# Kernel optimization log

Hardware: AMD Instinct MI355X
Metric: run time of the kernel (lower is better)

The kernel has to match this reference:

```python
import jax, jax.numpy as jnp
import numpy as np

N = 8192
D_IN = 512
D_OUT = 512


def setup_inputs() -> dict:
    key = jax.random.key(0)
    k1, k2, k3, k4 = jax.random.split(key, 4)
    x = jax.random.normal(k1, (N, D_IN), dtype=jnp.float32)
    adj = jax.random.uniform(k2, (N, N), dtype=jnp.float32)
    # nn.Linear params: weight (out, in), bias (out,)
    bound = 1.0 / np.sqrt(D_IN)
    W = jax.random.uniform(k3, (D_OUT, D_IN), minval=-bound, maxval=bound, dtype=jnp.float32)
    b = jax.random.uniform(k4, (D_OUT,), minval=-bound, maxval=bound, dtype=jnp.float32)
    return {"x": x, "adj": adj, "W": W, "b": b}


def reference(x, adj, W, b):
    # Symmetric normalization: D^-1/2 (A + I) D^-1/2.
    # Original uses diag-matmuls; broadcast scaling is the identical math
    # without the O(n^3) diagonal GEMMs.
    a = adj + jnp.eye(adj.shape[0], dtype=adj.dtype)
    d = jnp.sum(a, axis=1) ** -0.5  # (N,)
    a_norm = d[:, None] * a * d[None, :]
    support = a_norm @ x                      # (N, D_IN)
    out = support @ W.T + b                   # (N, D_OUT)
    out = jax.nn.relu(out)
    # dropout: identity in eval/reference mode
    return out
```

## Files before the change

### kernel.cpp

```cpp
#include <hip/hip_runtime.h>
#include <stdint.h>

typedef __bf16 bf16_t;
typedef __bf16 bf16x8 __attribute__((ext_vector_type(8)));
typedef __bf16 bf16x4v __attribute__((ext_vector_type(4)));
typedef float f32x16 __attribute__((ext_vector_type(16)));

#define AS_GLOBAL __attribute__((address_space(1)))
#define AS_LDS    __attribute__((address_space(3)))

static constexpr int NN   = 8192;
static constexpr int DIN  = 512;
static constexpr int DOUT = 512;
static constexpr int SPLITK = 2;

__device__ __forceinline__ void async_cp16(const bf16_t* g, bf16_t* l) {
  __builtin_amdgcn_global_load_lds((AS_GLOBAL unsigned int*)g,
                                   (AS_LDS unsigned int*)l, 16, 0, 0);
}

__global__ __launch_bounds__(256) void k_rowsum_convert(
    const float* __restrict__ adj, bf16_t* __restrict__ adjb,
    float* __restrict__ d) {
  const int row = blockIdx.x;
  const int t = threadIdx.x;
  const float4* rf4 = (const float4*)(adj + (size_t)row * NN);
  bf16_t* outp = adjb + (size_t)row * NN;
  float sum = 0.f;
#pragma unroll
  for (int c = 0; c < 8; ++c) {
    int f4i = c * 256 + t;
    float4 a = rf4[f4i];
    sum += a.x + a.y + a.z + a.w;
    bf16x4v o;
    o[0] = (bf16_t)a.x; o[1] = (bf16_t)a.y; o[2] = (bf16_t)a.z; o[3] = (bf16_t)a.w;
    *(bf16x4v*)(outp + f4i * 4) = o;
  }
#pragma unroll
  for (int off = 32; off > 0; off >>= 1) sum += __shfl_down(sum, off);
  __shared__ float red[4];
  if ((t & 63) == 0) red[t >> 6] = sum;
  __syncthreads();
  if (t == 0) {
    float s = red[0] + red[1] + red[2] + red[3] + 1.0f;
    d[row] = rsqrtf(s);
  }
}

__global__ __launch_bounds__(256) void k_make_xsT(
    const float* __restrict__ x, const float* __restrict__ d,
    bf16_t* __restrict__ xsT) {
  __shared__ bf16_t T[64][72];
  const int t = threadIdx.x;
  const int k0 = blockIdx.x * 64, j0 = blockIdx.y * 64;
#pragma unroll
  for (int it = 0; it < 4; ++it) {
    int idx = it * 256 + t;
    int r = idx >> 4, c = idx & 15;
    float4 v = *(const float4*)(x + (size_t)(k0 + r) * DIN + j0 + c * 4);
    float s = d[k0 + r];
    T[r][c * 4 + 0] = (bf16_t)(v.x * s);
    T[r][c * 4 + 1] = (bf16_t)(v.y * s);
    T[r][c * 4 + 2] = (bf16_t)(v.z * s);
    T[r][c * 4 + 3] = (bf16_t)(v.w * s);
  }
  __syncthreads();
#pragma unroll
  for (int it = 0; it < 2; ++it) {
    int idx = it * 256 + t;
    int j = idx >> 3, kb = idx & 7;
    bf16x8 o;
#pragma unroll
    for (int e = 0; e < 8; ++e) o[e] = T[kb * 8 + e][j];
    *(bf16x8*)(xsT + (size_t)(j0 + j) * NN + k0 + kb * 8) = o;
  }
}

__global__ __launch_bounds__(256) void k_convert_w(
    const float* __restrict__ W, bf16_t* __restrict__ Wb) {
  int idx = blockIdx.x * 256 + threadIdx.x;
  float4 v = *(const float4*)(W + (size_t)idx * 4);
  bf16x4v o;
  o[0] = (bf16_t)v.x; o[1] = (bf16_t)v.y; o[2] = (bf16_t)v.z; o[3] = (bf16_t)v.w;
  *(bf16x4v*)(Wb + (size_t)idx * 4) = o;
}

__device__ __forceinline__ void gemm_tile_128x128(
    const bf16_t* __restrict__ A, const bf16_t* __restrict__ B,
    int lda, int ldb, int m0, int n0, int kStart, int kEnd,
    bf16_t* As, bf16_t* Bs, f32x16 acc[2][2]) {
  const int t = threadIdx.x;
  const int lane = t & 63;
  const int wid = t >> 6;
  const int wm = wid >> 1, wn = wid & 1;
  const int l32 = lane & 31, half = lane >> 5;

  const int swz = (t & 7) ^ ((t >> 3) & 7);
  const bf16_t* gA = A + (size_t)(m0 + (t >> 3)) * lda + swz * 8 + kStart;
  const bf16_t* gB = B + (size_t)(n0 + (t >> 3)) * ldb + swz * 8 + kStart;
  bf16_t* lA = As + t * 8;
  bf16_t* lB = Bs + t * 8;

  const int xorc = lane & 7;

  for (int k0 = kStart; k0 < kEnd; k0 += 64) {
#pragma unroll
    for (int i = 0; i < 4; ++i) {
      async_cp16(gA + (size_t)(i * 32) * lda, lA + i * 2048);
      async_cp16(gB + (size_t)(i * 32) * ldb, lB + i * 2048);
    }
    gA += 64; gB += 64;
    __syncthreads();
#pragma unroll
    for (int ks = 0; ks < 4; ++ks) {
      const int pchunk = ((ks * 2 + half) ^ xorc) * 8;
      bf16x8 av[2], bv[2];
#pragma unroll
      for (int f = 0; f < 2; ++f) {
        av[f] = *(const bf16x8*)(As + (wm * 64 + f * 32 + l32) * 64 + pchunk);
        bv[f] = *(const bf16x8*)(Bs + (wn * 64 + f * 32 + l32) * 64 + pchunk);
      }
#pragma unroll
      for (int fm = 0; fm < 2; ++fm)
#pragma unroll
        for (int fn = 0; fn < 2; ++fn)
          acc[fm][fn] = __builtin_amdgcn_mfma_f32_32x32x16_bf16(
              av[fm], bv[fn], acc[fm][fn], 0, 0, 0);
    }
    __syncthreads();
  }
}

__global__ __launch_bounds__(256) void k_gemm1(
    const bf16_t* __restrict__ adjb, const bf16_t* __restrict__ xsT,
    float* __restrict__ part) {
  __shared__ bf16_t As[128 * 64];
  __shared__ bf16_t Bs[128 * 64];
  f32x16 acc[2][2];
#pragma unroll
  for (int a = 0; a < 2; ++a)
#pragma unroll
    for (int b = 0; b < 2; ++b)
#pragma unroll
      for (int r = 0; r < 16; ++r) acc[a][b][r] = 0.f;

  const int m0 = blockIdx.x * 128, n0 = blockIdx.y * 128;
  const int kc = blockIdx.z;
  const int kChunk = NN / SPLITK;
  gemm_tile_128x128(adjb, xsT, NN, NN, m0, n0, kc * kChunk, (kc + 1) * kChunk,
                    As, Bs, acc);

  const int t = threadIdx.x;
  const int lane = t & 63, wid = t >> 6;
  const int wm = wid >> 1, wn = wid & 1;
  const int l32 = lane & 31, half = lane >> 5;
  float* outp = part + (size_t)kc * NN * DIN;
#pragma unroll
  for (int fm = 0; fm < 2; ++fm)
#pragma unroll
    for (int fn = 0; fn < 2; ++fn) {
      int gc = n0 + wn * 64 + fn * 32 + l32;
#pragma unroll
      for (int reg = 0; reg < 16; ++reg) {
        int gr = m0 + wm * 64 + fm * 32 + (reg & 3) + 8 * (reg >> 2) + 4 * half;
        outp[(size_t)gr * DIN + gc] = acc[fm][fn][reg];
      }
    }
}

__global__ __launch_bounds__(256) void k_combine(
    const float* __restrict__ part, const float* __restrict__ d,
    const float* __restrict__ x, bf16_t* __restrict__ supB) {
  int idx = blockIdx.x * 256 + threadIdx.x;
  int i = idx >> 7;
  float4 p = *(const float4*)(part + (size_t)idx * 4);
#pragma unroll
  for (int kc = 1; kc < SPLITK; ++kc) {
    float4 q = *(const float4*)(part + (size_t)kc * NN * DIN + (size_t)idx * 4);
    p.x += q.x; p.y += q.y; p.z += q.z; p.w += q.w;
  }
  float4 xv = *(const float4*)(x + (size_t)idx * 4);
  float di = d[i];
  float dii = di * di;
  bf16x4v o;
  o[0] = (bf16_t)(di * p.x + dii * xv.x);
  o[1] = (bf16_t)(di * p.y + dii * xv.y);
  o[2] = (bf16_t)(di * p.z + dii * xv.z);
  o[3] = (bf16_t)(di * p.w + dii * xv.w);
  *(bf16x4v*)(supB + (size_t)idx * 4) = o;
}

__global__ __launch_bounds__(256) void k_gemm2(
    const bf16_t* __restrict__ supB, const bf16_t* __restrict__ Wb,
    const float* __restrict__ bias, float* __restrict__ outp) {
  __shared__ bf16_t As[128 * 64];
  __shared__ bf16_t Bs[128 * 64];
  f32x16 acc[2][2];
#pragma unroll
  for (int a = 0; a < 2; ++a)
#pragma unroll
    for (int b = 0; b < 2; ++b)
#pragma unroll
      for (int r = 0; r < 16; ++r) acc[a][b][r] = 0.f;

  const int m0 = blockIdx.x * 128, n0 = blockIdx.y * 128;
  gemm_tile_128x128(supB, Wb, DIN, DIN, m0, n0, 0, DIN, As, Bs, acc);

  const int t = threadIdx.x;
  const int lane = t & 63, wid = t >> 6;
  const int wm = wid >> 1, wn = wid & 1;
  const int l32 = lane & 31, half = lane >> 5;
#pragma unroll
  for (int fn = 0; fn < 2; ++fn) {
    int gc = n0 + wn * 64 + fn * 32 + l32;
    float bb = bias[gc];
#pragma unroll
    for (int fm = 0; fm < 2; ++fm)
#pragma unroll
      for (int reg = 0; reg < 16; ++reg) {
        int gr = m0 + wm * 64 + fm * 32 + (reg & 3) + 8 * (reg >> 2) + 4 * half;
        float v = acc[fm][fn][reg] + bb;
        outp[(size_t)gr * DOUT + gc] = v > 0.f ? v : 0.f;
      }
  }
}

extern "C" void kernel_launch(void* const* d_in, const int* in_sizes, int n_in,
                              void* d_out, int out_size, void* d_ws, size_t ws_size,
                              hipStream_t stream) {
  const float* x   = (const float*)d_in[0];
  const float* adj = (const float*)d_in[1];
  const float* W   = (const float*)d_in[2];
  const float* b   = (const float*)d_in[3];
  float* out = (float*)d_out;

  char* ws = (char*)d_ws;
  bf16_t* adjb = (bf16_t*)(ws);
  float*  part = (float*)(ws + 134217728);
  size_t  off  = 134217728 + (size_t)SPLITK * NN * DIN * 4;
  bf16_t* xsT  = (bf16_t*)(ws + off);
  bf16_t* supB = (bf16_t*)(ws + off + 8388608);
  bf16_t* Wb   = (bf16_t*)(ws + off + 16777216);
  float*  dvec = (float*)(ws + off + 17301504);

  k_rowsum_convert<<<NN, 256, 0, stream>>>(adj, adjb, dvec);
  k_make_xsT<<<dim3(NN / 64, DIN / 64), 256, 0, stream>>>(x, dvec, xsT);
  k_convert_w<<<(DOUT * DIN) / 1024, 256, 0, stream>>>(W, Wb);
  k_gemm1<<<dim3(NN / 128, DIN / 128, SPLITK), 256, 0, stream>>>(adjb, xsT, part);
  k_combine<<<(NN * DIN) / 1024, 256, 0, stream>>>(part, dvec, x, supB);
  k_gemm2<<<dim3(NN / 128, DOUT / 128), 256, 0, stream>>>(supB, Wb, b, out);
}
```

Baseline: 519.7 us.

## Reassociate GCN as A·(D·X·Wᵀ), fold identity into adj, double-buffer GEMM

Reorders the computation so X·Wᵀ, scaled by the degree vector, is computed first as a small GEMM. The result is written transposed and fed to the big adjacency GEMM. The identity diagonal is folded into the bf16 adjacency during conversion, and bias plus ReLU move into the split-K reduction kernel. This removes the separate x transpose kernel and the second N×512×512 GEMM over the support matrix. It also adds LDS double-buffering with explicit vmcnt waits to both GEMMs. The trade-off is that rounding now happens at different points and LDS use per block doubles.

```diff
diff --git a/kernel.cpp b/kernel.cpp
--- a/kernel.cpp
+++ b/kernel.cpp
@@ -26,6 +26,7 @@
   const int t = threadIdx.x;
   const float4* rf4 = (const float4*)(adj + (size_t)row * NN);
   bf16_t* outp = adjb + (size_t)row * NN;
+  const int diagF4 = row >> 2;
   float sum = 0.f;
 #pragma unroll
   for (int c = 0; c < 8; ++c) {
@@ -34,6 +35,11 @@
     sum += a.x + a.y + a.z + a.w;
     bf16x4v o;
     o[0] = (bf16_t)a.x; o[1] = (bf16_t)a.y; o[2] = (bf16_t)a.z; o[3] = (bf16_t)a.w;
+    if (f4i == diagF4) {
+      int s = row & 3;
+      float vv = s == 0 ? a.x : s == 1 ? a.y : s == 2 ? a.z : a.w;
+      o[s] = (bf16_t)(vv + 1.0f);
+    }
     *(bf16x4v*)(outp + f4i * 4) = o;
   }
 #pragma unroll
@@ -47,33 +53,17 @@
   }
 }
 
-__global__ __launch_bounds__(256) void k_make_xsT(
+__global__ __launch_bounds__(256) void k_dx(
     const float* __restrict__ x, const float* __restrict__ d,
-    bf16_t* __restrict__ xsT) {
-  __shared__ bf16_t T[64][72];
-  const int t = threadIdx.x;
-  const int k0 = blockIdx.x * 64, j0 = blockIdx.y * 64;
-#pragma unroll
-  for (int it = 0; it < 4; ++it) {
-    int idx = it * 256 + t;
-    int r = idx >> 4, c = idx & 15;
-    float4 v = *(const float4*)(x + (size_t)(k0 + r) * DIN + j0 + c * 4);
-    float s = d[k0 + r];
-    T[r][c * 4 + 0] = (bf16_t)(v.x * s);
-    T[r][c * 4 + 1] = (bf16_t)(v.y * s);
-    T[r][c * 4 + 2] = (bf16_t)(v.z * s);
-    T[r][c * 4 + 3] = (bf16_t)(v.w * s);
-  }
-  __syncthreads();
-#pragma unroll
-  for (int it = 0; it < 2; ++it) {
-    int idx = it * 256 + t;
-    int j = idx >> 3, kb = idx & 7;
-    bf16x8 o;
-#pragma unroll
-    for (int e = 0; e < 8; ++e) o[e] = T[kb * 8 + e][j];
-    *(bf16x8*)(xsT + (size_t)(j0 + j) * NN + k0 + kb * 8) = o;
-  }
+    bf16_t* __restrict__ dxb) {
+  int idx = blockIdx.x * 256 + threadIdx.x;
+  int i = idx >> 7;
+  float4 v = *(const float4*)(x + (size_t)idx * 4);
+  float s = d[i];
+  bf16x4v o;
+  o[0] = (bf16_t)(v.x * s); o[1] = (bf16_t)(v.y * s);
+  o[2] = (bf16_t)(v.z * s); o[3] = (bf16_t)(v.w * s);
+  *(bf16x4v*)(dxb + (size_t)idx * 4) = o;
 }
 
 __global__ __launch_bounds__(256) void k_convert_w(
@@ -85,7 +75,7 @@
   *(bf16x4v*)(Wb + (size_t)idx * 4) = o;
 }
 
-__device__ __forceinline__ void gemm_tile_128x128(
+__device__ __forceinline__ void gemm_tile_128x128_db(
     const bf16_t* __restrict__ A, const bf16_t* __restrict__ B,
     int lda, int ldb, int m0, int n0, int kStart, int kEnd,
     bf16_t* As, bf16_t* Bs, f32x16 acc[2][2]) {
@@ -98,27 +88,42 @@
   const int swz = (t & 7) ^ ((t >> 3) & 7);
   const bf16_t* gA = A + (size_t)(m0 + (t >> 3)) * lda + swz * 8 + kStart;
   const bf16_t* gB = B + (size_t)(n0 + (t >> 3)) * ldb + swz * 8 + kStart;
-  bf16_t* lA = As + t * 8;
-  bf16_t* lB = Bs + t * 8;
-
   const int xorc = lane & 7;
-
-  for (int k0 = kStart; k0 < kEnd; k0 += 64) {
-#pragma unroll
-    for (int i = 0; i < 4; ++i) {
-      async_cp16(gA + (size_t)(i * 32) * lda, lA + i * 2048);
-      async_cp16(gB + (size_t)(i * 32) * ldb, lB + i * 2048);
-    }
-    gA += 64; gB += 64;
-    __syncthreads();
+  const int nIter = (kEnd - kStart) >> 6;
+
+#pragma unroll
+  for (int i = 0; i < 4; ++i) {
+    async_cp16(gA + (size_t)(i * 32) * lda, As + t * 8 + i * 2048);
+    async_cp16(gB + (size_t)(i * 32) * ldb, Bs + t * 8 + i * 2048);
+  }
+  gA += 64; gB += 64;
+
+  int cur = 0;
+  for (int it = 0; it < nIter; ++it) {
+    if (it + 1 < nIter) {
+      const int nb = (cur ^ 1) * 8192;
+#pragma unroll
+      for (int i = 0; i < 4; ++i) {
+        async_cp16(gA + (size_t)(i * 32) * lda, As + nb + t * 8 + i * 2048);
+        async_cp16(gB + (size_t)(i * 32) * ldb, Bs + nb + t * 8 + i * 2048);
+      }
+      gA += 64; gB += 64;
+      asm volatile("s_waitcnt vmcnt(8)" ::: "memory");
+    } else {
+      asm volatile("s_waitcnt vmcnt(0)" ::: "memory");
+    }
+    __builtin_amdgcn_s_barrier();
+
+    const bf16_t* Ab = As + cur * 8192;
+    const bf16_t* Bb = Bs + cur * 8192;
 #pragma unroll
     for (int ks = 0; ks < 4; ++ks) {
       const int pchunk = ((ks * 2 + half) ^ xorc) * 8;
       bf16x8 av[2], bv[2];
 #pragma unroll
       for (int f = 0; f < 2; ++f) {
-        av[f] = *(const bf16x8*)(As + (wm * 64 + f * 32 + l32) * 64 + pchunk);
-        bv[f] = *(const bf16x8*)(Bs + (wn * 64 + f * 32 + l32) * 64 + pchunk);
+        av[f] = *(const bf16x8*)(Ab + (wm * 64 + f * 32 + l32) * 64 + pchunk);
+        bv[f] = *(const bf16x8*)(Bb + (wn * 64 + f * 32 + l32) * 64 + pchunk);
       }
 #pragma unroll
       for (int fm = 0; fm < 2; ++fm)
@@ -127,15 +132,50 @@
           acc[fm][fn] = __builtin_amdgcn_mfma_f32_32x32x16_bf16(
               av[fm], bv[fn], acc[fm][fn], 0, 0, 0);
     }
-    __syncthreads();
-  }
+    asm volatile("s_waitcnt lgkmcnt(0)" ::: "memory");
+    __builtin_amdgcn_s_barrier();
+    cur ^= 1;
+  }
+}
+
+__global__ __launch_bounds__(256) void k_gemmY(
+    const bf16_t* __restrict__ Wb, const bf16_t* __restrict__ dxb,
+    bf16_t* __restrict__ YT) {
+  __shared__ __align__(16) bf16_t As[2 * 128 * 64];
+  __shared__ __align__(16) bf16_t Bs[2 * 128 * 64];
+  f32x16 acc[2][2];
+#pragma unroll
+  for (int a = 0; a < 2; ++a)
+#pragma unroll
+    for (int b = 0; b < 2; ++b)
+#pragma unroll
+      for (int r = 0; r < 16; ++r) acc[a][b][r] = 0.f;
+
+  const int m0 = blockIdx.x * 128, n0 = blockIdx.y * 128;
+  gemm_tile_128x128_db(Wb, dxb, DIN, DIN, m0, n0, 0, DIN, As, Bs, acc);
+
+  const int t = threadIdx.x;
+  const int lane = t & 63, wid = t >> 6;
+  const int wm = wid >> 1, wn = wid & 1;
+  const int l32 = lane & 31, half = lane >> 5;
+#pragma unroll
+  for (int fm = 0; fm < 2; ++fm)
+#pragma unroll
+    for (int fn = 0; fn < 2; ++fn) {
+      int gc = n0 + wn * 64 + fn * 32 + l32;
+#pragma unroll
+      for (int reg = 0; reg < 16; ++reg) {
+        int gr = m0 + wm * 64 + fm * 32 + (reg & 3) + 8 * (reg >> 2) + 4 * half;
+        YT[(size_t)gr * NN + gc] = (bf16_t)acc[fm][fn][reg];
+      }
+    }
 }
 
 __global__ __launch_bounds__(256) void k_gemm1(
-    const bf16_t* __restrict__ adjb, const bf16_t* __restrict__ xsT,
+    const bf16_t* __restrict__ adjb, const bf16_t* __restrict__ YT,
     float* __restrict__ part) {
-  __shared__ bf16_t As[128 * 64];
-  __shared__ bf16_t Bs[128 * 64];
+  __shared__ __align__(16) bf16_t As[2 * 128 * 64];
+  __shared__ __align__(16) bf16_t Bs[2 * 128 * 64];
   f32x16 acc[2][2];
 #pragma unroll
   for (int a = 0; a < 2; ++a)
@@ -147,14 +187,14 @@
   const int m0 = blockIdx.x * 128, n0 = blockIdx.y * 128;
   const int kc = blockIdx.z;
   const int kChunk = NN / SPLITK;
-  gemm_tile_128x128(adjb, xsT, NN, NN, m0, n0, kc * kChunk, (kc + 1) * kChunk,
-                    As, Bs, acc);
+  gemm_tile_128x128_db(adjb, YT, NN, NN, m0, n0, kc * kChunk, (kc + 1) * kChunk,
+                       As, Bs, acc);
 
   const int t = threadIdx.x;
   const int lane = t & 63, wid = t >> 6;
   const int wm = wid >> 1, wn = wid & 1;
   const int l32 = lane & 31, half = lane >> 5;
-  float* outp = part + (size_t)kc * NN * DIN;
+  float* outp = part + (size_t)kc * NN * DOUT;
 #pragma unroll
   for (int fm = 0; fm < 2; ++fm)
 #pragma unroll
@@ -163,66 +203,31 @@
 #pragma unroll
       for (int reg = 0; reg < 16; ++reg) {
         int gr = m0 + wm * 64 + fm * 32 + (reg & 3) + 8 * (reg >> 2) + 4 * half;
-        outp[(size_t)gr * DIN + gc] = acc[fm][fn][reg];
-      }
-    }
-}
-
-__global__ __launch_bounds__(256) void k_combine(
+        outp[(size_t)gr * DOUT + gc] = acc[fm][fn][reg];
+      }
+    }
+}
+
+__global__ __launch_bounds__(256) void k_out(
     const float* __restrict__ part, const float* __restrict__ d,
-    const float* __restrict__ x, bf16_t* __restrict__ supB) {
+    const float* __restrict__ bias, float* __restrict__ outp) {
   int idx = blockIdx.x * 256 + threadIdx.x;
   int i = idx >> 7;
+  int j4 = idx & 127;
   float4 p = *(const float4*)(part + (size_t)idx * 4);
 #pragma unroll
   for (int kc = 1; kc < SPLITK; ++kc) {
-    float4 q = *(const float4*)(part + (size_t)kc * NN * DIN + (size_t)idx * 4);
+    float4 q = *(const float4*)(part + (size_t)kc * NN * DOUT + (size_t)idx * 4);
     p.x += q.x; p.y += q.y; p.z += q.z; p.w += q.w;
   }
-  float4 xv = *(const float4*)(x + (size_t)idx * 4);
+  float4 bb = *(const float4*)(bias + j4 * 4);
   float di = d[i];
-  float dii = di * di;
-  bf16x4v o;
-  o[0] = (bf16_t)(di * p.x + dii * xv.x);
-  o[1] = (bf16_t)(di * p.y + dii * xv.y);
-  o[2] = (bf16_t)(di * p.z + dii * xv.z);
-  o[3] = (bf16_t)(di * p.w + dii * xv.w);
-  *(bf16x4v*)(supB + (size_t)idx * 4) = o;
-}
-
-__global__ __launch_bounds__(256) void k_gemm2(
-    const bf16_t* __restrict__ supB, const bf16_t* __restrict__ Wb,
-    const float* __restrict__ bias, float* __restrict__ outp) {
-  __shared__ bf16_t As[128 * 64];
-  __shared__ bf16_t Bs[128 * 64];
-  f32x16 acc[2][2];
-#pragma unroll
-  for (int a = 0; a < 2; ++a)
-#pragma unroll
-    for (int b = 0; b < 2; ++b)
-#pragma unroll
-      for (int r = 0; r < 16; ++r) acc[a][b][r] = 0.f;
-
-  const int m0 = blockIdx.x * 128, n0 = blockIdx.y * 128;
-  gemm_tile_128x128(supB, Wb, DIN, DIN, m0, n0, 0, DIN, As, Bs, acc);
-
-  const int t = threadIdx.x;
-  const int lane = t & 63, wid = t >> 6;
-  const int wm = wid >> 1, wn = wid & 1;
-  const int l32 = lane & 31, half = lane >> 5;
-#pragma unroll
-  for (int fn = 0; fn < 2; ++fn) {
-    int gc = n0 + wn * 64 + fn * 32 + l32;
-    float bb = bias[gc];
-#pragma unroll
-    for (int fm = 0; fm < 2; ++fm)
-#pragma unroll
-      for (int reg = 0; reg < 16; ++reg) {
-        int gr = m0 + wm * 64 + fm * 32 + (reg & 3) + 8 * (reg >> 2) + 4 * half;
-        float v = acc[fm][fn][reg] + bb;
-        outp[(size_t)gr * DOUT + gc] = v > 0.f ? v : 0.f;
-      }
-  }
+  float4 o;
+  o.x = fmaxf(fmaf(di, p.x, bb.x), 0.f);
+  o.y = fmaxf(fmaf(di, p.y, bb.y), 0.f);
+  o.z = fmaxf(fmaf(di, p.z, bb.z), 0.f);
+  o.w = fmaxf(fmaf(di, p.w, bb.w), 0.f);
+  *(float4*)(outp + (size_t)idx * 4) = o;
 }
 
 extern "C" void kernel_launch(void* const* d_in, const int* in_sizes, int n_in,
@@ -237,16 +242,15 @@
   char* ws = (char*)d_ws;
   bf16_t* adjb = (bf16_t*)(ws);
   float*  part = (float*)(ws + 134217728);
-  size_t  off  = 134217728 + (size_t)SPLITK * NN * DIN * 4;
-  bf16_t* xsT  = (bf16_t*)(ws + off);
-  bf16_t* supB = (bf16_t*)(ws + off + 8388608);
-  bf16_t* Wb   = (bf16_t*)(ws + off + 16777216);
-  float*  dvec = (float*)(ws + off + 17301504);
+  bf16_t* YT   = (bf16_t*)(ws + 167772160);
+  bf16_t* dxb  = (bf16_t*)(ws + 176160768);
+  bf16_t* Wb   = (bf16_t*)(ws + 184549376);
+  float*  dvec = (float*)(ws + 185073664);
 
   k_rowsum_convert<<<NN, 256, 0, stream>>>(adj, adjb, dvec);
-  k_make_xsT<<<dim3(NN / 64, DIN / 64), 256, 0, stream>>>(x, dvec, xsT);
+  k_dx<<<(NN * DIN) / 1024, 256, 0, stream>>>(x, dvec, dxb);
   k_convert_w<<<(DOUT * DIN) / 1024, 256, 0, stream>>>(W, Wb);
-  k_gemm1<<<dim3(NN / 128, DIN / 128, SPLITK), 256, 0, stream>>>(adjb, xsT, part);
-  k_combine<<<(NN * DIN) / 1024, 256, 0, stream>>>(part, dvec, x, supB);
-  k_gemm2<<<dim3(NN / 128, DOUT / 128), 256, 0, stream>>>(supB, Wb, b, out);
-}
+  k_gemmY<<<dim3(DOUT / 128, NN / 128), 256, 0, stream>>>(Wb, dxb, YT);
+  k_gemm1<<<dim3(NN / 128, DOUT / 128, SPLITK), 256, 0, stream>>>(adjb, YT, part);
+  k_out<<<(NN * DOUT) / 1024, 256, 0, stream>>>(part, dvec, b, out);
+}
```

Measured after the change: 512.8 us. About the same (-1.3%).
